# Kernel optimization log

Hardware: AMD Instinct MI355X
Metric: run time of the kernel (lower is better)

Reference implementation:

```python
import jax, jax.numpy as jnp
import numpy as np

B, S, D, H, M = 4, 1024, 1024, 16, 128
HD = D // H  # 64


def setup_inputs() -> dict:
    key = jax.random.key(0)
    ks = jax.random.split(key, 12)
    s = 0.02
    return {
        "x": jax.random.normal(ks[0], (B, S, D), dtype=jnp.float32),
        "Wq": jax.random.normal(ks[1], (D, D), dtype=jnp.float32) * s,
        "bq": jnp.zeros((D,), dtype=jnp.float32),
        "Wk": jax.random.normal(ks[2], (D, D), dtype=jnp.float32) * s,
        "bk": jnp.zeros((D,), dtype=jnp.float32),
        "Wv": jax.random.normal(ks[3], (D, D), dtype=jnp.float32) * s,
        "bv": jnp.zeros((D,), dtype=jnp.float32),
        "Wo": jax.random.normal(ks[4], (D, D), dtype=jnp.float32) * s,
        "bo": jnp.zeros((D,), dtype=jnp.float32),
        "u": jax.random.normal(ks[5], (H, HD), dtype=jnp.float32) * s,
        "v": jax.random.normal(ks[6], (H, HD), dtype=jnp.float32) * s,
    }


def _rel_sinusoid_emb():
    # [2M+1, HD] sinusoidal embeddings over relative offsets -M..M
    rel_range = jnp.arange(-M, M + 1, dtype=jnp.float32)
    inv_freq = 1.0 / (10000.0 ** (jnp.arange(0, HD, 2, dtype=jnp.float32) / HD))
    sinusoid = rel_range[:, None] * inv_freq[None, :]  # [2M+1, HD/2]
    emb = jnp.zeros((2 * M + 1, HD), dtype=jnp.float32)
    emb = emb.at[:, 0::2].set(jnp.sin(sinusoid))
    emb = emb.at[:, 1::2].set(jnp.cos(sinusoid))
    return emb


def reference(x, Wq, bq, Wk, bk, Wv, bv, Wo, bo, u, v):
    scale = 1.0 / np.sqrt(HD).astype(np.float32)

    def heads(t):  # [B,S,D] -> [B,H,S,HD]
        return t.reshape(B, S, H, HD).transpose(0, 2, 1, 3)

    q = heads(x @ Wq + bq)
    k = heads(x @ Wk + bk)
    vv = heads(x @ Wv + bv)

    rel_emb = _rel_sinusoid_emb()  # [2M+1, HD]
    pos = jnp.arange(S)
    rel_index = jnp.clip(pos[None, :] - pos[:, None], -M, M) + M  # [S,S] int

    q_u = q + u[None, :, None, :]
    q_v = q + v[None, :, None, :]

    content = jnp.einsum("bhid,bhjd->bhij", q_u, k) * scale  # [B,H,S,S]
    # einsum('bhid,ijd->bhij', q_v, rel_emb[rel_index]) == gather of per-bucket scores
    rel_all = jnp.einsum("bhid,rd->bhir", q_v, rel_emb) * scale  # [B,H,S,2M+1]
    rel_scores = jnp.take_along_axis(rel_all, rel_index[None, None, :, :], axis=-1)

    attn = jax.nn.softmax(content + rel_scores, axis=-1)
    out = jnp.einsum("bhij,bhjd->bhid", attn, vv)  # [B,H,S,HD]
    out = out.transpose(0, 2, 1, 3).reshape(B, S, D)
    return out @ Wo + bo
```

## Files before the change

### kernel.cpp

```cpp
#include <hip/hip_runtime.h>
#include <math.h>


#define BB 4
#define SS 1024
#define DD 1024
#define HH 16
#define HDIM 64
#define SCALE 0.125f
#define KMAX_BOUND 16.0f

typedef __attribute__((ext_vector_type(8))) short short8;
typedef __attribute__((ext_vector_type(4))) float f32x4;
typedef __attribute__((ext_vector_type(4))) unsigned short us4;
typedef unsigned short u16;

#define MFMA __builtin_amdgcn_mfma_f32_16x16x32_bf16

__device__ __forceinline__ float b2f(u16 v) {
  return __uint_as_float((unsigned)v << 16);
}
__device__ __forceinline__ u16 f2b(float f) {
  unsigned u = __float_as_uint(f);
  return (u16)((u + 0x7FFF + ((u >> 16) & 1)) >> 16);
}
__device__ __forceinline__ void gl_lds16(const u16* g, u16* l) {
  __builtin_amdgcn_global_load_lds(
      (const __attribute__((address_space(1))) unsigned int*)(g),
      (__attribute__((address_space(3))) unsigned int*)(l), 16, 0, 0);
}

__global__ __launch_bounds__(256) void prep(
    const float* __restrict__ x,
    const float* __restrict__ W0, const float* __restrict__ W1,
    const float* __restrict__ W2, const float* __restrict__ W3,
    u16* __restrict__ xb,
    u16* __restrict__ T0, u16* __restrict__ T1,
    u16* __restrict__ T2, u16* __restrict__ T3,
    u16* __restrict__ Eb) {
  __shared__ float t[64 * 68];
  const int bid = blockIdx.x, tid = threadIdx.x;
  if (bid < 2048) {
    const size_t i = ((size_t)bid * 256 + tid) * 8;
    float4 a = *reinterpret_cast<const float4*>(&x[i]);
    float4 b = *reinterpret_cast<const float4*>(&x[i + 4]);
    short8 v;
    v[0] = (short)f2b(a.x); v[1] = (short)f2b(a.y);
    v[2] = (short)f2b(a.z); v[3] = (short)f2b(a.w);
    v[4] = (short)f2b(b.x); v[5] = (short)f2b(b.y);
    v[6] = (short)f2b(b.z); v[7] = (short)f2b(b.w);
    *reinterpret_cast<short8*>(&xb[i]) = v;
  } else if (bid < 3072) {
    const int wz = bid - 2048;
    const int z = wz >> 8;
    const float* W = z == 0 ? W0 : z == 1 ? W1 : z == 2 ? W2 : W3;
    u16* T = z == 0 ? T0 : z == 1 ? T1 : z == 2 ? T2 : T3;
    const int k0 = ((wz >> 4) & 15) * 64, n0 = (wz & 15) * 64;
#pragma unroll
    for (int rd = 0; rd < 4; ++rd) {
      const int idx = rd * 256 + tid;
      const int r = idx >> 4, c4 = (idx & 15) * 4;
      *reinterpret_cast<float4*>(&t[r * 68 + c4]) =
          *reinterpret_cast<const float4*>(&W[(size_t)(k0 + r) * DD + n0 + c4]);
    }
    __syncthreads();
#pragma unroll
    for (int rd = 0; rd < 2; ++rd) {
      const int idx = rd * 256 + tid;
      const int rr = idx >> 3, cc = (idx & 7) * 8;
      short8 v;
#pragma unroll
      for (int e = 0; e < 8; ++e) v[e] = (short)f2b(t[(cc + e) * 68 + rr]);
      *reinterpret_cast<short8*>(&T[(size_t)(n0 + rr) * DD + k0 + cc]) = v;
    }
  } else {
    const int j = (bid - 3072) * 4 + (tid >> 6);
    const int d = tid & 63;
    const int pair = d >> 1;
    const float inv_freq =
        exp2f(-((float)(2 * pair) / 64.0f) * 13.287712379549449f);
    const float arg = (float)j * inv_freq;
    const float val = (d & 1) ? cosf(arg) : sinf(arg);
    Eb[j * 64 + d] = f2b(val);
  }
}

__global__ __launch_bounds__(256, 3) void gemm_mfma(
    const u16* __restrict__ A,
    const u16* __restrict__ W0, const u16* __restrict__ W1, const u16* __restrict__ W2,
    const float* __restrict__ b0, const float* __restrict__ b1, const float* __restrict__ b2,
    void* o0, void* o1, void* o2, int final_mode) {
  const int z = blockIdx.z;
  const u16* Bt = z == 0 ? W0 : z == 1 ? W1 : W2;
  const float* bias = z == 0 ? b0 : z == 1 ? b1 : b2;
  __shared__ u16 As0[128 * 32];
  __shared__ u16 Bs0[128 * 32];
  __shared__ u16 As1[128 * 32];
  __shared__ u16 Bs1[128 * 32];
  const int tid = threadIdx.x;
  const int bm = blockIdx.y * 128, bn = blockIdx.x * 128;
  const int lane = tid & 63, w = tid >> 6;
  const int wr = w >> 1, wc = w & 1;
  const int lr = lane & 15, lg = lane >> 4;

  const int r_i0 = 32 * w + (lane >> 2);
  const int r_i1 = r_i0 + 16;
  const int q0 = (lane & 3) ^ ((r_i0 >> 1) & 3);
  const int q1 = (lane & 3) ^ ((r_i1 >> 1) & 3);
  const u16* gA0 = &A[(size_t)(bm + r_i0) * DD + q0 * 8];
  const u16* gA1 = &A[(size_t)(bm + r_i1) * DD + q1 * 8];
  const u16* gB0 = &Bt[(size_t)(bn + r_i0) * DD + q0 * 8];
  const u16* gB1 = &Bt[(size_t)(bn + r_i1) * DD + q1 * 8];
  const int lo0 = (32 * w) * 32;
  const int lo1 = (32 * w + 16) * 32;

  const f32x4 Z4 = {0.f, 0.f, 0.f, 0.f};
  f32x4 acc[4][4];
#pragma unroll
  for (int m = 0; m < 4; ++m)
#pragma unroll
    for (int n = 0; n < 4; ++n) acc[m][n] = Z4;

  auto STAGE = [&](u16* Ab, u16* Bb, int kk) {
    gl_lds16(gA0 + kk, Ab + lo0);
    gl_lds16(gA1 + kk, Ab + lo1);
    gl_lds16(gB0 + kk, Bb + lo0);
    gl_lds16(gB1 + kk, Bb + lo1);
  };
  auto COMPUTE = [&](u16* Ab, u16* Bb) {
    short8 af[4], bf[4];
#pragma unroll
    for (int m = 0; m < 4; ++m) {
      const int row = wr * 64 + m * 16 + lr;
      af[m] = *reinterpret_cast<short8*>(&Ab[row * 32 + ((lg ^ ((row >> 1) & 3)) * 8)]);
    }
#pragma unroll
    for (int n = 0; n < 4; ++n) {
      const int row = wc * 64 + n * 16 + lr;
      bf[n] = *reinterpret_cast<short8*>(&Bb[row * 32 + ((lg ^ ((row >> 1) & 3)) * 8)]);
    }
#pragma unroll
    for (int m = 0; m < 4; ++m)
#pragma unroll
      for (int n = 0; n < 4; ++n)
        acc[m][n] = MFMA(af[m], bf[n], acc[m][n], 0, 0, 0);
  };

  STAGE(As0, Bs0, 0);
  __syncthreads();
  for (int k0 = 0; k0 < DD; k0 += 64) {
    STAGE(As1, Bs1, k0 + 32);
    COMPUTE(As0, Bs0);
    __syncthreads();
    if (k0 + 64 < DD) STAGE(As0, Bs0, k0 + 64);
    COMPUTE(As1, Bs1);
    __syncthreads();
  }

  const int mode = final_mode ? 2 : (z == 2 ? 1 : 0);
  u16* ob = (u16*)(z == 0 ? o0 : z == 1 ? o1 : o2);
  float* of = (float*)o0;
#pragma unroll
  for (int m = 0; m < 4; ++m) {
#pragma unroll
    for (int n = 0; n < 4; ++n) {
      const int col = bn + wc * 64 + n * 16 + lr;
      const float bv = bias[col];
      const int row0 = bm + wr * 64 + m * 16 + lg * 4;
      if (mode == 0) {
#pragma unroll
        for (int g = 0; g < 4; ++g)
          ob[(size_t)(row0 + g) * DD + col] = f2b(acc[m][n][g] + bv);
      } else if (mode == 2) {
#pragma unroll
        for (int g = 0; g < 4; ++g)
          of[(size_t)(row0 + g) * DD + col] = acc[m][n][g] + bv;
      } else {
        const int bI = row0 >> 10, s0 = row0 & 1023;
        us4 pk;
#pragma unroll
        for (int g = 0; g < 4; ++g) pk[g] = f2b(acc[m][n][g] + bv);
        *reinterpret_cast<us4*>(&ob[(size_t)col * 4096 + bI * 1024 + s0]) = pk;
      }
    }
  }
}

__global__ __launch_bounds__(256, 3) void attn_mfma(
    const u16* __restrict__ Qg, const u16* __restrict__ Kg,
    const u16* __restrict__ Vtg, const u16* __restrict__ Eb,
    const float* __restrict__ ub, const float* __restrict__ vb,
    u16* __restrict__ AO) {
  __shared__ u16 kk_l[64 * 128];
  __shared__ u16 vt_l[64 * 64];
  __shared__ u16 ps_l[128 * 64];
  __shared__ float ls_l[128];

  const int tid = threadIdx.x;
  const int it = blockIdx.x, h = blockIdx.y, b = blockIdx.z;
  const int i0 = it * 128;
  const int lane = tid & 63, w = tid >> 6;
  const int lr = lane & 15, lg = lane >> 4;
  const f32x4 Z4 = {0.f, 0.f, 0.f, 0.f};

  short8 aq[2][4];
  float Mrow[2], cL[2], cR[2];
#pragma unroll
  for (int m = 0; m < 2; ++m) {
    const int qpos = i0 + w * 32 + m * 16 + lr;
    const size_t qbase = (size_t)(b * SS + qpos) * DD + h * 64;
    const int iL = qpos >= 128 ? qpos - 128 : 0;
    const int iR = qpos <= 895 ? qpos + 128 : 1023;
    float nqu = 0.f, nqv = 0.f, clp = 0.f, crp = 0.f;
#pragma unroll
    for (int ks2 = 0; ks2 < 2; ++ks2) {
      const int d8 = ks2 * 32 + lg * 8;
      short8 q8 = *reinterpret_cast<const short8*>(&Qg[qbase + d8]);
      short8 e8 = *reinterpret_cast<const short8*>(&Eb[qpos * 64 + d8]);
      short8 eL8 = *reinterpret_cast<const short8*>(&Eb[iL * 64 + d8]);
      short8 eR8 = *reinterpret_cast<const short8*>(&Eb[iR * 64 + d8]);
      float us[8], vs[8];
      {
        float4 a = *reinterpret_cast<const float4*>(&ub[h * 64 + d8]);
        float4 d = *reinterpret_cast<const float4*>(&ub[h * 64 + d8 + 4]);
        us[0] = a.x; us[1] = a.y; us[2] = a.z; us[3] = a.w;
        us[4] = d.x; us[5] = d.y; us[6] = d.z; us[7] = d.w;
        float4 e = *reinterpret_cast<const float4*>(&vb[h * 64 + d8]);
        float4 f = *reinterpret_cast<const float4*>(&vb[h * 64 + d8 + 4]);
        vs[0] = e.x; vs[1] = e.y; vs[2] = e.z; vs[3] = e.w;
        vs[4] = f.x; vs[5] = f.y; vs[6] = f.z; vs[7] = f.w;
      }
      short8 xu, xr;
#pragma unroll
      for (int e = 0; e < 8; ++e) {
        const float qf = b2f((u16)q8[e]);
        xu[e] = (short)f2b(qf + us[e]);
        const float quf = b2f((u16)xu[e]);
        nqu = fmaf(quf, quf, nqu);
      }
#pragma unroll
      for (int p = 0; p < 4; ++p) {
        const float qv0 = b2f((u16)q8[2 * p]) + vs[2 * p];
        const float qv1 = b2f((u16)q8[2 * p + 1]) + vs[2 * p + 1];
        const float si = b2f((u16)e8[2 * p]), co = b2f((u16)e8[2 * p + 1]);
        const float r0 = qv0 * co + qv1 * si;
        const float r1 = qv1 * co - qv0 * si;
        xr[2 * p] = (short)f2b(r0);
        xr[2 * p + 1] = (short)f2b(r1);
        const float a0 = b2f((u16)xr[2 * p]), a1 = b2f((u16)xr[2 * p + 1]);
        nqv = fmaf(a0, a0, fmaf(a1, a1, nqv));
        clp = fmaf(a0, b2f((u16)eL8[2 * p]), fmaf(a1, b2f((u16)eL8[2 * p + 1]), clp));
        crp = fmaf(a0, b2f((u16)eR8[2 * p]), fmaf(a1, b2f((u16)eR8[2 * p + 1]), crp));
      }
      aq[m][ks2] = xu;
      aq[m][ks2 + 2] = xr;
    }
    nqu += __shfl_xor(nqu, 16); nqu += __shfl_xor(nqu, 32);
    nqv += __shfl_xor(nqv, 16); nqv += __shfl_xor(nqv, 32);
    clp += __shfl_xor(clp, 16); clp += __shfl_xor(clp, 32);
    crp += __shfl_xor(crp, 16); crp += __shfl_xor(crp, 32);
    Mrow[m] = 0.125f * KMAX_BOUND * sqrtf(nqu) + 0.7125f * sqrtf(nqv) + 0.03f;
    cL[m] = 0.125f * clp;
    cR[m] = 0.125f * crp;
  }

  float lsum[2] = {0.f, 0.f};
  f32x4 o_acc[2][4];
#pragma unroll
  for (int nq = 0; nq < 2; ++nq)
#pragma unroll
    for (int df = 0; df < 4; ++df) o_acc[nq][df] = Z4;

  const int srow = tid >> 2, sc4 = tid & 3;
  const int vr = tid >> 3, vc = tid & 7;
  const size_t kcol = (size_t)h * 64 + sc4 * 16;

  short8 kA, kB, eA, eB, v0r, v1r;
  {
    const size_t kbase = (size_t)(b * SS + srow) * DD + kcol;
    kA = *reinterpret_cast<const short8*>(&Kg[kbase]);
    kB = *reinterpret_cast<const short8*>(&Kg[kbase + 8]);
    const size_t ebase = (size_t)srow * 64 + sc4 * 16;
    eA = *reinterpret_cast<const short8*>(&Eb[ebase]);
    eB = *reinterpret_cast<const short8*>(&Eb[ebase + 8]);
    v0r = *reinterpret_cast<const short8*>(
        &Vtg[(size_t)(h * 64 + vr) * 4096 + b * SS + vc * 8]);
    v1r = *reinterpret_cast<const short8*>(
        &Vtg[(size_t)(h * 64 + vr + 32) * 4096 + b * SS + vc * 8]);
  }

  for (int jt = 0; jt < 16; ++jt) {
    const int j0 = jt * 64;
    __syncthreads();
    {
      const int rs = srow & 15;
      *reinterpret_cast<short8*>(&kk_l[srow * 128 + (((sc4 * 2) ^ rs) * 8)]) = kA;
      *reinterpret_cast<short8*>(&kk_l[srow * 128 + (((sc4 * 2 + 1) ^ rs) * 8)]) = kB;
      *reinterpret_cast<short8*>(&kk_l[srow * 128 + (((8 + sc4 * 2) ^ rs) * 8)]) = eA;
      *reinterpret_cast<short8*>(&kk_l[srow * 128 + (((9 + sc4 * 2) ^ rs) * 8)]) = eB;
      *reinterpret_cast<short8*>(&vt_l[vr * 64 + ((vc ^ (vr & 7)) * 8)]) = v0r;
      *reinterpret_cast<short8*>(&vt_l[(vr + 32) * 64 + ((vc ^ ((vr + 32) & 7)) * 8)]) = v1r;
    }
    __syncthreads();

    if (jt < 15) {
      const int jn = j0 + 64;
      const size_t kbase = (size_t)(b * SS + jn + srow) * DD + kcol;
      kA = *reinterpret_cast<const short8*>(&Kg[kbase]);
      kB = *reinterpret_cast<const short8*>(&Kg[kbase + 8]);
      const size_t ebase = (size_t)(jn + srow) * 64 + sc4 * 16;
      eA = *reinterpret_cast<const short8*>(&Eb[ebase]);
      eB = *reinterpret_cast<const short8*>(&Eb[ebase + 8]);
      v0r = *reinterpret_cast<const short8*>(
          &Vtg[(size_t)(h * 64 + vr) * 4096 + b * SS + jn + vc * 8]);
      v1r = *reinterpret_cast<const short8*>(
          &Vtg[(size_t)(h * 64 + vr + 32) * 4096 + b * SS + jn + vc * 8]);
    }

    const int roW = j0 - i0 - w * 32;
    if (roW < -191 || roW > 159) {
      const float fb0 = (roW < 0 ? cL[0] : cR[0]) - Mrow[0];
      const float fb1 = (roW < 0 ? cL[1] : cR[1]) - Mrow[1];
#pragma unroll
      for (int nf = 0; nf < 4; ++nf) {
        const int krow = nf * 16 + lr;
        short8 kf0 = *reinterpret_cast<short8*>(
            &kk_l[krow * 128 + ((lg ^ lr) * 8)]);
        short8 kf1 = *reinterpret_cast<short8*>(
            &kk_l[krow * 128 + (((4 + lg) ^ lr) * 8)]);
#pragma unroll
        for (int nq = 0; nq < 2; ++nq) {
          f32x4 s = MFMA(kf0, aq[nq][0], Z4, 0, 0, 0);
          s = MFMA(kf1, aq[nq][1], s, 0, 0, 0);
          const float base = nq == 0 ? fb0 : fb1;
          us4 pk;
#pragma unroll
          for (int g = 0; g < 4; ++g) {
            const float p = __expf(fmaf(s[g], SCALE, base));
            lsum[nq] += p;
            pk[g] = f2b(p);
          }
          const int prow = w * 32 + nq * 16 + lr;
          *reinterpret_cast<us4*>(
              &ps_l[prow * 64 + (((nf * 2 + (lg >> 1)) ^ (prow & 7)) * 8) +
                    4 * (lg & 1)]) = pk;
        }
      }
    } else {
#pragma unroll
      for (int nf = 0; nf < 4; ++nf) {
        const int krow = nf * 16 + lr;
        short8 kf0 = *reinterpret_cast<short8*>(
            &kk_l[krow * 128 + ((lg ^ lr) * 8)]);
        short8 kf1 = *reinterpret_cast<short8*>(
            &kk_l[krow * 128 + (((4 + lg) ^ lr) * 8)]);
        short8 kf2 = *reinterpret_cast<short8*>(
            &kk_l[krow * 128 + (((8 + lg) ^ lr) * 8)]);
        short8 kf3 = *reinterpret_cast<short8*>(
            &kk_l[krow * 128 + (((12 + lg) ^ lr) * 8)]);
#pragma unroll
        for (int nq = 0; nq < 2; ++nq) {
          f32x4 c = MFMA(kf0, aq[nq][0], Z4, 0, 0, 0);
          c = MFMA(kf1, aq[nq][1], c, 0, 0, 0);
          f32x4 t = MFMA(kf2, aq[nq][2], c, 0, 0, 0);
          t = MFMA(kf3, aq[nq][3], t, 0, 0, 0);
          const int rob = roW + nf * 16 + lg * 4 - nq * 16 - lr;
          const float bI = -Mrow[nq];
          const float bL = cL[nq] - Mrow[nq];
          const float bR = cR[nq] - Mrow[nq];
          us4 pk;
#pragma unroll
          for (int g = 0; g < 4; ++g) {
            const int ro = rob + g;
            const bool inr = (ro >= -128) && (ro <= 128);
            const float sval = inr ? t[g] : c[g];
            const float base = inr ? bI : (ro < -128 ? bL : bR);
            const float p = __expf(fmaf(sval, SCALE, base));
            lsum[nq] += p;
            pk[g] = f2b(p);
          }
          const int prow = w * 32 + nq * 16 + lr;
          *reinterpret_cast<us4*>(
              &ps_l[prow * 64 + (((nf * 2 + (lg >> 1)) ^ (prow & 7)) * 8) +
                    4 * (lg & 1)]) = pk;
        }
      }
    }

#pragma unroll
    for (int ks = 0; ks < 2; ++ks) {
      short8 ap0, ap1;
      {
        const int r0q = w * 32 + lr;
        ap0 = *reinterpret_cast<short8*>(
            &ps_l[r0q * 64 + (((ks * 4 + lg) ^ (r0q & 7)) * 8)]);
        const int r1q = w * 32 + 16 + lr;
        ap1 = *reinterpret_cast<short8*>(
            &ps_l[r1q * 64 + (((ks * 4 + lg) ^ (r1q & 7)) * 8)]);
      }
#pragma unroll
      for (int df = 0; df < 4; ++df) {
        const int vrow = df * 16 + lr;
        short8 vf = *reinterpret_cast<short8*>(
            &vt_l[vrow * 64 + (((ks * 4 + lg) ^ (vrow & 7)) * 8)]);
        o_acc[0][df] = MFMA(ap0, vf, o_acc[0][df], 0, 0, 0);
        o_acc[1][df] = MFMA(ap1, vf, o_acc[1][df], 0, 0, 0);
      }
    }
  }

#pragma unroll
  for (int nq = 0; nq < 2; ++nq) {
    lsum[nq] += __shfl_xor(lsum[nq], 16);
    lsum[nq] += __shfl_xor(lsum[nq], 32);
    ls_l[w * 32 + nq * 16 + lr] = lsum[nq];
  }
#pragma unroll
  for (int nq = 0; nq < 2; ++nq) {
#pragma unroll
    for (int g = 0; g < 4; ++g) {
      const float inv = 1.0f / ls_l[w * 32 + nq * 16 + lg * 4 + g];
      const int row = b * SS + i0 + w * 32 + nq * 16 + lg * 4 + g;
#pragma unroll
      for (int df = 0; df < 4; ++df) {
        AO[(size_t)row * DD + h * 64 + df * 16 + lr] =
            f2b(o_acc[nq][df][g] * inv);
      }
    }
  }
}

extern "C" void kernel_launch(void* const* d_in, const int* in_sizes, int n_in,
                              void* d_out, int out_size, void* d_ws, size_t ws_size,
                              hipStream_t stream) {
  const float* x  = (const float*)d_in[0];
  const float* Wq = (const float*)d_in[1];
  const float* bq = (const float*)d_in[2];
  const float* Wk = (const float*)d_in[3];
  const float* bk = (const float*)d_in[4];
  const float* Wv = (const float*)d_in[5];
  const float* bv = (const float*)d_in[6];
  const float* Wo = (const float*)d_in[7];
  const float* bo = (const float*)d_in[8];
  const float* u  = (const float*)d_in[9];
  const float* v  = (const float*)d_in[10];
  float* out = (float*)d_out;

  char* p = (char*)d_ws;
  const size_t TOK = (size_t)4096 * 1024 * 2;
  const size_t WSZ = (size_t)1024 * 1024 * 2;
  u16* Eb   = (u16*)p; p += (size_t)1024 * 64 * 2;
  u16* xb   = (u16*)p; p += TOK;
  u16* Wqt  = (u16*)p; p += WSZ;
  u16* Wkt  = (u16*)p; p += WSZ;
  u16* Wvt  = (u16*)p; p += WSZ;
  u16* Wot  = (u16*)p; p += WSZ;
  u16* Qb   = (u16*)p; p += TOK;
  u16* Kb   = (u16*)p; p += TOK;
  u16* Vt   = (u16*)p; p += TOK;
  u16* AOb  = (u16*)p; p += TOK;

  prep<<<3328, 256, 0, stream>>>(x, Wq, Wk, Wv, Wo, xb, Wqt, Wkt, Wvt, Wot, Eb);

  gemm_mfma<<<dim3(8, 32, 3), 256, 0, stream>>>(
      xb, Wqt, Wkt, Wvt, bq, bk, bv, Qb, Kb, Vt, 0);

  attn_mfma<<<dim3(SS / 128, HH, BB), 256, 0, stream>>>(
      Qb, Kb, Vt, Eb, u, v, AOb);

  gemm_mfma<<<dim3(8, 32, 1), 256, 0, stream>>>(
      AOb, Wot, Wot, Wot, bo, bo, bo, out, out, out, 1);
}
```

Before: 109.4 us.

## Fuse x fp32-to-bf16 conversion into QKV GEMM, drop K/V prefetch, use exp2

The separate prep pass that converted x to bf16 is removed. The QKV GEMM now loads fp32 x rows into registers, converts them, and writes them into swizzled LDS, which saves a full write and read of the bf16 activation buffer. The attention kernel drops its register prefetch of the next K/E/V tile, loading each tile at the top of the iteration instead. It also folds log2(e) into the softmax bias so it can call exp2f. The fused A path adds conversion work and register pressure inside the GEMM loop, and losing the prefetch may expose global load latency in attention.

```diff
diff --git a/kernel.cpp b/kernel.cpp
--- a/kernel.cpp
+++ b/kernel.cpp
@@ -8,6 +8,8 @@
 #define HH 16
 #define HDIM 64
 #define SCALE 0.125f
+#define LOG2E 1.4426950408889634f
+#define SC2 (0.125f * LOG2E)
 #define KMAX_BOUND 16.0f
 
 typedef __attribute__((ext_vector_type(8))) short short8;
@@ -31,27 +33,15 @@
 }
 
 __global__ __launch_bounds__(256) void prep(
-    const float* __restrict__ x,
     const float* __restrict__ W0, const float* __restrict__ W1,
     const float* __restrict__ W2, const float* __restrict__ W3,
-    u16* __restrict__ xb,
     u16* __restrict__ T0, u16* __restrict__ T1,
     u16* __restrict__ T2, u16* __restrict__ T3,
     u16* __restrict__ Eb) {
   __shared__ float t[64 * 68];
   const int bid = blockIdx.x, tid = threadIdx.x;
-  if (bid < 2048) {
-    const size_t i = ((size_t)bid * 256 + tid) * 8;
-    float4 a = *reinterpret_cast<const float4*>(&x[i]);
-    float4 b = *reinterpret_cast<const float4*>(&x[i + 4]);
-    short8 v;
-    v[0] = (short)f2b(a.x); v[1] = (short)f2b(a.y);
-    v[2] = (short)f2b(a.z); v[3] = (short)f2b(a.w);
-    v[4] = (short)f2b(b.x); v[5] = (short)f2b(b.y);
-    v[6] = (short)f2b(b.z); v[7] = (short)f2b(b.w);
-    *reinterpret_cast<short8*>(&xb[i]) = v;
-  } else if (bid < 3072) {
-    const int wz = bid - 2048;
+  if (bid < 1024) {
+    const int wz = bid;
     const int z = wz >> 8;
     const float* W = z == 0 ? W0 : z == 1 ? W1 : z == 2 ? W2 : W3;
     u16* T = z == 0 ? T0 : z == 1 ? T1 : z == 2 ? T2 : T3;
@@ -74,7 +64,7 @@
       *reinterpret_cast<short8*>(&T[(size_t)(n0 + rr) * DD + k0 + cc]) = v;
     }
   } else {
-    const int j = (bid - 3072) * 4 + (tid >> 6);
+    const int j = (bid - 1024) * 4 + (tid >> 6);
     const int d = tid & 63;
     const int pair = d >> 1;
     const float inv_freq =
@@ -86,7 +76,7 @@
 }
 
 __global__ __launch_bounds__(256, 3) void gemm_mfma(
-    const u16* __restrict__ A,
+    const float* __restrict__ Af, const u16* __restrict__ A,
     const u16* __restrict__ W0, const u16* __restrict__ W1, const u16* __restrict__ W2,
     const float* __restrict__ b0, const float* __restrict__ b1, const float* __restrict__ b2,
     void* o0, void* o1, void* o2, int final_mode) {
@@ -105,14 +95,20 @@
 
   const int r_i0 = 32 * w + (lane >> 2);
   const int r_i1 = r_i0 + 16;
-  const int q0 = (lane & 3) ^ ((r_i0 >> 1) & 3);
-  const int q1 = (lane & 3) ^ ((r_i1 >> 1) & 3);
+  const int c4l = lane & 3;
+  const int q0 = c4l ^ ((r_i0 >> 1) & 3);
+  const int q1 = c4l ^ ((r_i1 >> 1) & 3);
   const u16* gA0 = &A[(size_t)(bm + r_i0) * DD + q0 * 8];
   const u16* gA1 = &A[(size_t)(bm + r_i1) * DD + q1 * 8];
+  const float* fA0 = &Af[(size_t)(bm + r_i0) * DD + c4l * 8];
+  const float* fA1 = &Af[(size_t)(bm + r_i1) * DD + c4l * 8];
   const u16* gB0 = &Bt[(size_t)(bn + r_i0) * DD + q0 * 8];
   const u16* gB1 = &Bt[(size_t)(bn + r_i1) * DD + q1 * 8];
   const int lo0 = (32 * w) * 32;
   const int lo1 = (32 * w + 16) * 32;
+  const int aw0 = r_i0 * 32 + (c4l ^ ((r_i0 >> 1) & 3)) * 8;
+  const int aw1 = r_i1 * 32 + (c4l ^ ((r_i1 >> 1) & 3)) * 8;
+  const bool af32 = (final_mode == 0);
 
   const f32x4 Z4 = {0.f, 0.f, 0.f, 0.f};
   f32x4 acc[4][4];
@@ -121,9 +117,31 @@
 #pragma unroll
     for (int n = 0; n < 4; ++n) acc[m][n] = Z4;
 
-  auto STAGE = [&](u16* Ab, u16* Bb, int kk) {
+  float4 ar[4];
+  auto ALOAD = [&](int kk) {
+    ar[0] = *reinterpret_cast<const float4*>(fA0 + kk);
+    ar[1] = *reinterpret_cast<const float4*>(fA0 + kk + 4);
+    ar[2] = *reinterpret_cast<const float4*>(fA1 + kk);
+    ar[3] = *reinterpret_cast<const float4*>(fA1 + kk + 4);
+  };
+  auto AWRITE = [&](u16* Ab) {
+    short8 v0, v1;
+    v0[0] = (short)f2b(ar[0].x); v0[1] = (short)f2b(ar[0].y);
+    v0[2] = (short)f2b(ar[0].z); v0[3] = (short)f2b(ar[0].w);
+    v0[4] = (short)f2b(ar[1].x); v0[5] = (short)f2b(ar[1].y);
+    v0[6] = (short)f2b(ar[1].z); v0[7] = (short)f2b(ar[1].w);
+    v1[0] = (short)f2b(ar[2].x); v1[1] = (short)f2b(ar[2].y);
+    v1[2] = (short)f2b(ar[2].z); v1[3] = (short)f2b(ar[2].w);
+    v1[4] = (short)f2b(ar[3].x); v1[5] = (short)f2b(ar[3].y);
+    v1[6] = (short)f2b(ar[3].z); v1[7] = (short)f2b(ar[3].w);
+    *reinterpret_cast<short8*>(&Ab[aw0]) = v0;
+    *reinterpret_cast<short8*>(&Ab[aw1]) = v1;
+  };
+  auto STAGE_A_LDS = [&](u16* Ab, int kk) {
     gl_lds16(gA0 + kk, Ab + lo0);
     gl_lds16(gA1 + kk, Ab + lo1);
+  };
+  auto STAGE_B = [&](u16* Bb, int kk) {
     gl_lds16(gB0 + kk, Bb + lo0);
     gl_lds16(gB1 + kk, Bb + lo1);
   };
@@ -146,14 +164,21 @@
         acc[m][n] = MFMA(af[m], bf[n], acc[m][n], 0, 0, 0);
   };
 
-  STAGE(As0, Bs0, 0);
+  if (af32) { ALOAD(0); AWRITE(As0); } else { STAGE_A_LDS(As0, 0); }
+  STAGE_B(Bs0, 0);
   __syncthreads();
   for (int k0 = 0; k0 < DD; k0 += 64) {
-    STAGE(As1, Bs1, k0 + 32);
+    if (af32) ALOAD(k0 + 32); else STAGE_A_LDS(As1, k0 + 32);
+    STAGE_B(Bs1, k0 + 32);
     COMPUTE(As0, Bs0);
+    if (af32) AWRITE(As1);
     __syncthreads();
-    if (k0 + 64 < DD) STAGE(As0, Bs0, k0 + 64);
+    if (k0 + 64 < DD) {
+      if (af32) ALOAD(k0 + 64); else STAGE_A_LDS(As0, k0 + 64);
+      STAGE_B(Bs0, k0 + 64);
+    }
     COMPUTE(As1, Bs1);
+    if (af32 && k0 + 64 < DD) AWRITE(As0);
     __syncthreads();
   }
 
@@ -204,7 +229,7 @@
   const f32x4 Z4 = {0.f, 0.f, 0.f, 0.f};
 
   short8 aq[2][4];
-  float Mrow[2], cL[2], cR[2];
+  float bI2[2], bL2[2], bR2[2];
 #pragma unroll
   for (int m = 0; m < 2; ++m) {
     const int qpos = i0 + w * 32 + m * 16 + lr;
@@ -259,9 +284,11 @@
     nqv += __shfl_xor(nqv, 16); nqv += __shfl_xor(nqv, 32);
     clp += __shfl_xor(clp, 16); clp += __shfl_xor(clp, 32);
     crp += __shfl_xor(crp, 16); crp += __shfl_xor(crp, 32);
-    Mrow[m] = 0.125f * KMAX_BOUND * sqrtf(nqu) + 0.7125f * sqrtf(nqv) + 0.03f;
-    cL[m] = 0.125f * clp;
-    cR[m] = 0.125f * crp;
+    const float Mrow =
+        0.125f * KMAX_BOUND * sqrtf(nqu) + 0.7125f * sqrtf(nqv) + 0.03f;
+    bI2[m] = -Mrow * LOG2E;
+    bL2[m] = (0.125f * clp - Mrow) * LOG2E;
+    bR2[m] = (0.125f * crp - Mrow) * LOG2E;
   }
 
   float lsum[2] = {0.f, 0.f};
@@ -273,24 +300,19 @@
 
   const int srow = tid >> 2, sc4 = tid & 3;
   const int vr = tid >> 3, vc = tid & 7;
-  const size_t kcol = (size_t)h * 64 + sc4 * 16;
-
-  short8 kA, kB, eA, eB, v0r, v1r;
-  {
-    const size_t kbase = (size_t)(b * SS + srow) * DD + kcol;
-    kA = *reinterpret_cast<const short8*>(&Kg[kbase]);
-    kB = *reinterpret_cast<const short8*>(&Kg[kbase + 8]);
-    const size_t ebase = (size_t)srow * 64 + sc4 * 16;
-    eA = *reinterpret_cast<const short8*>(&Eb[ebase]);
-    eB = *reinterpret_cast<const short8*>(&Eb[ebase + 8]);
-    v0r = *reinterpret_cast<const short8*>(
-        &Vtg[(size_t)(h * 64 + vr) * 4096 + b * SS + vc * 8]);
-    v1r = *reinterpret_cast<const short8*>(
-        &Vtg[(size_t)(h * 64 + vr + 32) * 4096 + b * SS + vc * 8]);
-  }
 
   for (int jt = 0; jt < 16; ++jt) {
     const int j0 = jt * 64;
+    const size_t kbase = (size_t)(b * SS + j0 + srow) * DD + h * 64 + sc4 * 16;
+    short8 kA = *reinterpret_cast<const short8*>(&Kg[kbase]);
+    short8 kB = *reinterpret_cast<const short8*>(&Kg[kbase + 8]);
+    const size_t ebase = (size_t)(j0 + srow) * 64 + sc4 * 16;
+    short8 eA = *reinterpret_cast<const short8*>(&Eb[ebase]);
+    short8 eB = *reinterpret_cast<const short8*>(&Eb[ebase + 8]);
+    short8 v0r = *reinterpret_cast<const short8*>(
+        &Vtg[(size_t)(h * 64 + vr) * 4096 + b * SS + j0 + vc * 8]);
+    short8 v1r = *reinterpret_cast<const short8*>(
+        &Vtg[(size_t)(h * 64 + vr + 32) * 4096 + b * SS + j0 + vc * 8]);
     __syncthreads();
     {
       const int rs = srow & 15;
@@ -303,24 +325,10 @@
     }
     __syncthreads();
 
-    if (jt < 15) {
-      const int jn = j0 + 64;
-      const size_t kbase = (size_t)(b * SS + jn + srow) * DD + kcol;
-      kA = *reinterpret_cast<const short8*>(&Kg[kbase]);
-      kB = *reinterpret_cast<const short8*>(&Kg[kbase + 8]);
-      const size_t ebase = (size_t)(jn + srow) * 64 + sc4 * 16;
-      eA = *reinterpret_cast<const short8*>(&Eb[ebase]);
-      eB = *reinterpret_cast<const short8*>(&Eb[ebase + 8]);
-      v0r = *reinterpret_cast<const short8*>(
-          &Vtg[(size_t)(h * 64 + vr) * 4096 + b * SS + jn + vc * 8]);
-      v1r = *reinterpret_cast<const short8*>(
-          &Vtg[(size_t)(h * 64 + vr + 32) * 4096 + b * SS + jn + vc * 8]);
-    }
-
     const int roW = j0 - i0 - w * 32;
     if (roW < -191 || roW > 159) {
-      const float fb0 = (roW < 0 ? cL[0] : cR[0]) - Mrow[0];
-      const float fb1 = (roW < 0 ? cL[1] : cR[1]) - Mrow[1];
+      const float fb0 = roW < 0 ? bL2[0] : bR2[0];
+      const float fb1 = roW < 0 ? bL2[1] : bR2[1];
 #pragma unroll
       for (int nf = 0; nf < 4; ++nf) {
         const int krow = nf * 16 + lr;
@@ -336,7 +344,7 @@
           us4 pk;
 #pragma unroll
           for (int g = 0; g < 4; ++g) {
-            const float p = __expf(fmaf(s[g], SCALE, base));
+            const float p = exp2f(fmaf(s[g], SC2, base));
             lsum[nq] += p;
             pk[g] = f2b(p);
           }
@@ -365,17 +373,14 @@
           f32x4 t = MFMA(kf2, aq[nq][2], c, 0, 0, 0);
           t = MFMA(kf3, aq[nq][3], t, 0, 0, 0);
           const int rob = roW + nf * 16 + lg * 4 - nq * 16 - lr;
-          const float bI = -Mrow[nq];
-          const float bL = cL[nq] - Mrow[nq];
-          const float bR = cR[nq] - Mrow[nq];
           us4 pk;
 #pragma unroll
           for (int g = 0; g < 4; ++g) {
             const int ro = rob + g;
             const bool inr = (ro >= -128) && (ro <= 128);
             const float sval = inr ? t[g] : c[g];
-            const float base = inr ? bI : (ro < -128 ? bL : bR);
-            const float p = __expf(fmaf(sval, SCALE, base));
+            const float base = inr ? bI2[nq] : (ro < -128 ? bL2[nq] : bR2[nq]);
+            const float p = exp2f(fmaf(sval, SC2, base));
             lsum[nq] += p;
             pk[g] = f2b(p);
           }
@@ -450,7 +455,6 @@
   const size_t TOK = (size_t)4096 * 1024 * 2;
   const size_t WSZ = (size_t)1024 * 1024 * 2;
   u16* Eb   = (u16*)p; p += (size_t)1024 * 64 * 2;
-  u16* xb   = (u16*)p; p += TOK;
   u16* Wqt  = (u16*)p; p += WSZ;
   u16* Wkt  = (u16*)p; p += WSZ;
   u16* Wvt  = (u16*)p; p += WSZ;
@@ -460,14 +464,14 @@
   u16* Vt   = (u16*)p; p += TOK;
   u16* AOb  = (u16*)p; p += TOK;
 
-  prep<<<3328, 256, 0, stream>>>(x, Wq, Wk, Wv, Wo, xb, Wqt, Wkt, Wvt, Wot, Eb);
+  prep<<<1280, 256, 0, stream>>>(Wq, Wk, Wv, Wo, Wqt, Wkt, Wvt, Wot, Eb);
 
   gemm_mfma<<<dim3(8, 32, 3), 256, 0, stream>>>(
-      xb, Wqt, Wkt, Wvt, bq, bk, bv, Qb, Kb, Vt, 0);
+      x, nullptr, Wqt, Wkt, Wvt, bq, bk, bv, Qb, Kb, Vt, 0);
 
   attn_mfma<<<dim3(SS / 128, HH, BB), 256, 0, stream>>>(
       Qb, Kb, Vt, Eb, u, v, AOb);
 
   gemm_mfma<<<dim3(8, 32, 1), 256, 0, stream>>>(
-      AOb, Wot, Wot, Wot, bo, bo, bo, out, out, out, 1);
-}
+      nullptr, AOb, Wot, Wot, Wot, bo, bo, bo, out, out, out, 1);
+}
```

Result: slower. 129.1 us (+18.0%).
